# Kernel optimization log

Hardware: AMD Instinct MI355X
Metric: run time of the kernel (lower is better)

## Reference

```python
import jax, jax.numpy as jnp
import numpy as np

ALPHA = 0.2  # leaky relu slope
NEG_INF = -9e15

B, N, F_IN, F_OUT = 2, 4096, 256, 256
EMB = 16  # int(sqrt(256))


def setup_inputs() -> dict:
    key = jax.random.key(0)
    ks = jax.random.split(key, 16)
    g = 1.414

    def xavier(k, shape):
        fan_in, fan_out = shape[0], shape[1]
        limit = g * np.sqrt(6.0 / (fan_in + fan_out))
        return jax.random.uniform(k, shape, jnp.float32, -limit, limit)

    feat = jax.random.normal(ks[0], (B, N, F_IN), jnp.float32)
    adj = jax.random.randint(ks[1], (B, N, N), 0, 2, jnp.int32)
    W = xavier(ks[2], (F_IN, F_OUT))
    a1 = xavier(ks[3], (F_OUT, 1))
    a2 = xavier(ks[4], (F_OUT, 1))
    a12 = xavier(ks[5], (F_OUT, F_OUT))
    # BiInteraction linear layers stored as [in, out] (= torch weight.T)
    def lin(k1, k2, fi, fo):
        lim = 1.0 / np.sqrt(fi)
        w = jax.random.uniform(k1, (fi, fo), jnp.float32, -lim, lim)
        b = jax.random.uniform(k2, (fo,), jnp.float32, -lim, lim)
        return w, b

    e1_w, e1_b = lin(ks[6], ks[7], F_IN, EMB)
    e2_w, e2_b = lin(ks[8], ks[9], F_IN, EMB)
    i0_w, i0_b = lin(ks[10], ks[11], 2 * EMB, F_OUT)
    i1_w, i1_b = lin(ks[12], ks[13], F_OUT, F_OUT)
    return {"feat": feat, "adj": adj, "W": W, "a1": a1, "a2": a2,
            "a12": a12, "e1_w": e1_w, "e1_b": e1_b, "e2_w": e2_w,
            "e2_b": e2_b, "i0_w": i0_w, "i0_b": i0_b, "i1_w": i1_w,
            "i1_b": i1_b}


def reference(feat, adj, W, a1, a2, a12, e1_w, e1_b, e2_w, e2_b,
              i0_w, i0_b, i1_w, i1_b):
    lrelu = lambda x: jax.nn.leaky_relu(x, ALPHA)
    # attention scores: logits[b,i,j] = a1.h_j + a2.h_i + h_i A12 h_j
    h = feat @ W                                   # [B,N,F_OUT]
    Ax = (h @ a1).transpose(0, 2, 1)               # [B,1,N] (key term)
    Ay = h @ a2                                    # [B,N,1] (query term)
    Axy = jnp.einsum('bnd,de,bme->bnm', h, a12, h) # [B,N,N] bilinear
    e = lrelu(Ax + Ay + Axy)
    e = jnp.where(adj > 0, e, NEG_INF)
    attention = jax.nn.softmax(e, axis=-1)         # masked softmax over j
    h_prime = attention @ feat                     # [B,N,F_IN]
    # BiInteraction MLP update
    emb1 = lrelu(feat @ e1_w + e1_b)
    emb2 = lrelu(h_prime @ e2_w + e2_b)
    c = jnp.concatenate([emb1, emb2], axis=-1)     # [B,N,2*EMB]
    c = lrelu(c @ i0_w + i0_b)
    c = lrelu(c @ i1_w + i1_b)
    return c
```

## Files before the change

kernel.cpp:

```cpp
#include <hip/hip_runtime.h>
#include <hip/hip_bf16.h>

typedef __attribute__((ext_vector_type(8))) __bf16 bf16x8;
typedef __attribute__((ext_vector_type(8))) short short8;
typedef __attribute__((ext_vector_type(4))) float floatx4;
typedef __attribute__((ext_vector_type(4))) int intx4;
typedef unsigned short u16;
typedef unsigned int u32;
typedef unsigned long long u64;

constexpr int BB = 2, NN = 4096, DD = 256;
constexpr int NCHUNK = 4;
constexpr int KSTEP = 32;
constexpr int CHUNKLEN = NN / NCHUNK;
constexpr int STEPS = CHUNKLEN / KSTEP;
constexpr float SLOPE = 0.2f;
constexpr float NEGINF = -9e15f;

#define DEVI static __device__ __forceinline__

DEVI u16 f2bf(float f) {
  u32 u = __float_as_uint(f);
  u += 0x7fffu + ((u >> 16) & 1u);
  return (u16)(u >> 16);
}
DEVI float bf2f(u16 h) { return __uint_as_float(((u32)h) << 16); }
DEVI float lrelu(float x) { return x > 0.f ? x : SLOPE * x; }

DEVI floatx4 mfma16(short8 a, short8 b, floatx4 c) {
  return __builtin_amdgcn_mfma_f32_16x16x32_bf16(
      __builtin_bit_cast(bf16x8, a), __builtin_bit_cast(bf16x8, b), c, 0, 0, 0);
}

__global__ void k_prep_w(const float* W, const float* A12, const float* I1,
                         u16* WThi, u16* WTlo, u16* A12Thi, u16* A12Tlo,
                         u16* I1Thi, u16* I1Tlo) {
  __shared__ float tile[32][33];
  const float* src = blockIdx.z == 0 ? W : (blockIdx.z == 1 ? A12 : I1);
  u16* dhi = blockIdx.z == 0 ? WThi : (blockIdx.z == 1 ? A12Thi : I1Thi);
  u16* dlo = blockIdx.z == 0 ? WTlo : (blockIdx.z == 1 ? A12Tlo : I1Tlo);
  int k0 = blockIdx.x * 32, n0 = blockIdx.y * 32;
  int tx = threadIdx.x, ty = threadIdx.y;
  #pragma unroll
  for (int r = 0; r < 4; r++)
    tile[ty + r * 8][tx] = src[(size_t)(k0 + ty + r * 8) * 256 + n0 + tx];
  __syncthreads();
  #pragma unroll
  for (int r = 0; r < 4; r++) {
    float v = tile[tx][ty + r * 8];
    u16 hb = f2bf(v);
    size_t o = (size_t)(n0 + ty + r * 8) * 256 + k0 + tx;
    dhi[o] = hb;
    dlo[o] = f2bf(v - bf2f(hb));
  }
}

__global__ void k_prep_e(const float* e1w, const float* e2w, float* e1t,
                         float* e2t) {
  int t = threadIdx.x;
  const float* src = blockIdx.x == 0 ? e1w : e2w;
  float* dst = blockIdx.x == 0 ? e1t : e2t;
  float v[16];
  #pragma unroll
  for (int o = 0; o < 16; o++) v[o] = src[t * 16 + o];
  #pragma unroll
  for (int o = 0; o < 16; o++) dst[o * 256 + t] = v[o];
}

__global__ void k_adjpack(const int* adj, u64* maskp) {
  int wave = (blockIdx.x * 256 + threadIdx.x) >> 6;
  int lane = threadIdx.x & 63;
  size_t base = (size_t)wave * 256;
  const int* p = adj + base;
  u64 m[4];
  #pragma unroll
  for (int r = 0; r < 4; r++) {
    int v = p[r * 64 + lane];
    m[r] = __ballot(v > 0);
  }
  if (lane < 4) {
    u64 sel = lane == 0 ? m[0] : lane == 1 ? m[1] : lane == 2 ? m[2] : m[3];
    maskp[base / 64 + lane] = sel;
  }
}

template <int AMODE, int EPI>
__global__ __launch_bounds__(256) void k_gemm(
    const float* Af32, const u16* Ahi, const u16* Alo,
    const u16* BThi, const u16* BTlo,
    u16* Ohi, u16* Olo, float* Of32, const float* bias) {
  int t = threadIdx.x;
  int wid = t >> 6, lane = t & 63;
  int li = lane & 15, lg = lane >> 4;
  int row0 = blockIdx.x * 64 + wid * 16;
  int col0 = blockIdx.y * 32;
  int arow = row0 + li;

  __shared__ __align__(16) u16 Bh[32 * 256];
  __shared__ __align__(16) u16 Bl[32 * 256];
  #pragma unroll
  for (int s = 0; s < 4; s++) {
    int r = s * 8 + (t >> 5), c8 = (t & 31) * 8;
    int off = r * 256 + (c8 ^ ((r & 7) << 3));
    *(intx4*)(Bh + off) = *(const intx4*)(BThi + (size_t)(col0 + r) * DD + c8);
    *(intx4*)(Bl + off) = *(const intx4*)(BTlo + (size_t)(col0 + r) * DD + c8);
  }

  short8 ahi[8], alo[8];
  if constexpr (AMODE == 0) {
    const float* ap = Af32 + (size_t)arow * DD + lg * 8;
    #pragma unroll
    for (int ks = 0; ks < 8; ks++) {
      floatx4 f0 = *(const floatx4*)(ap + ks * 32);
      floatx4 f1 = *(const floatx4*)(ap + ks * 32 + 4);
      short8 h, l;
      #pragma unroll
      for (int e = 0; e < 4; e++) {
        u16 hb = f2bf(f0[e]); h[e] = (short)hb; l[e] = (short)f2bf(f0[e] - bf2f(hb));
        u16 hb2 = f2bf(f1[e]); h[e + 4] = (short)hb2; l[e + 4] = (short)f2bf(f1[e] - bf2f(hb2));
      }
      ahi[ks] = h; alo[ks] = l;
    }
  } else {
    const u16* ap = Ahi + (size_t)arow * DD + lg * 8;
    const u16* ap2 = Alo + (size_t)arow * DD + lg * 8;
    #pragma unroll
    for (int ks = 0; ks < 8; ks++) {
      ahi[ks] = *(const short8*)(ap + ks * 32);
      alo[ks] = *(const short8*)(ap2 + ks * 32);
    }
  }
  __syncthreads();

  floatx4 acc[2];
  #pragma unroll
  for (int cf = 0; cf < 2; cf++) acc[cf] = 0.f;

  #pragma unroll
  for (int cf = 0; cf < 2; cf++) {
    int row = cf * 16 + li;
    int rsw = (row & 7) << 3;
    #pragma unroll
    for (int ks = 0; ks < 8; ks++) {
      int off = row * 256 + ((ks * 32 + lg * 8) ^ rsw);
      short8 bhf = *(const short8*)(Bh + off);
      short8 blf = *(const short8*)(Bl + off);
      acc[cf] = mfma16(ahi[ks], bhf, acc[cf]);
      acc[cf] = mfma16(alo[ks], bhf, acc[cf]);
      acc[cf] = mfma16(ahi[ks], blf, acc[cf]);
    }
  }

  #pragma unroll
  for (int cf = 0; cf < 2; cf++) {
    int col = col0 + cf * 16 + li;
    #pragma unroll
    for (int r = 0; r < 4; r++) {
      int row = row0 + lg * 4 + r;
      float v = acc[cf][r];
      if constexpr (EPI == 0) {
        u16 hb = f2bf(v);
        Ohi[(size_t)row * DD + col] = hb;
        Olo[(size_t)row * DD + col] = f2bf(v - bf2f(hb));
      } else {
        v += bias[col];
        v = lrelu(v);
        Of32[(size_t)row * DD + col] = v;
      }
    }
  }
}

__global__ void k_axay(const u16* h_hi, const u16* h_lo, const float* a1,
                       const float* a2, float* ax, float* ay) {
  int row = blockIdx.x * 4 + (threadIdx.x >> 6);
  int lane = threadIdx.x & 63;
  ushort4 hw = *(const ushort4*)(h_hi + (size_t)row * DD + lane * 4);
  ushort4 lw = *(const ushort4*)(h_lo + (size_t)row * DD + lane * 4);
  floatx4 av1 = *(const floatx4*)(a1 + lane * 4);
  floatx4 av2 = *(const floatx4*)(a2 + lane * 4);
  const u16* hp = (const u16*)&hw;
  const u16* lp = (const u16*)&lw;
  float s1 = 0.f, s2 = 0.f;
  #pragma unroll
  for (int r = 0; r < 4; r++) {
    float hv = bf2f(hp[r]) + bf2f(lp[r]);
    s1 += hv * av1[r];
    s2 += hv * av2[r];
  }
  #pragma unroll
  for (int off = 32; off; off >>= 1) {
    s1 += __shfl_xor(s1, off);
    s2 += __shfl_xor(s2, off);
  }
  if (lane == 0) { ax[row] = s1; ay[row] = s2; }
}

__global__ void k_featT(const float* feat, u16* featT) {
  __shared__ float tile[64][65];
  int b = blockIdx.z, n0 = blockIdx.x * 64, d0 = blockIdx.y * 64;
  int tx = threadIdx.x & 63, ty = threadIdx.x >> 6;
  #pragma unroll
  for (int r = 0; r < 16; r++) {
    int n = ty + r * 4;
    tile[n][tx] = feat[((size_t)b * NN + n0 + n) * DD + d0 + tx];
  }
  __syncthreads();
  #pragma unroll
  for (int r = 0; r < 16; r++) {
    int d = ty + r * 4;
    featT[((size_t)b * DD + d0 + d) * NN + n0 + tx] = f2bf(tile[tx][d]);
  }
}

__global__ __launch_bounds__(256, 2) void k_flash(
    const u16* t_hi, const u16* t_lo, const u16* h_hi, const u16* h_lo,
    const u16* featT, const float* ax, const float* ay, const u64* maskp,
    float* PO, float* m_ws, float* l_ws) {
  int id = blockIdx.x;
  int wg = (id & 7) * 64 + (id >> 3);
  int b = wg >> 8;
  int rem = wg & 255;
  int chunk = rem >> 6;
  int it = rem & 63;

  int t = threadIdx.x;
  int wid = t >> 6, lane = t & 63;
  int li = lane & 15, lg = lane >> 4;
  int i = it * 64 + wid * 16 + li;
  size_t browQ = (size_t)b * NN + i;

  __shared__ __align__(16) u16 Kh[KSTEP * 256];
  __shared__ __align__(16) u16 Kl[KSTEP * 256];
  __shared__ __align__(16) u16 Vs[256 * KSTEP];
  __shared__ __align__(16) u16 Pbuf[4][16][40];

  short8 qhi[8], qlo[8];
  {
    const u16* qp = t_hi + browQ * DD + lg * 8;
    const u16* qp2 = t_lo + browQ * DD + lg * 8;
    #pragma unroll
    for (int ks = 0; ks < 8; ks++) {
      qhi[ks] = *(const short8*)(qp + ks * 32);
      qlo[ks] = *(const short8*)(qp2 + ks * 32);
    }
  }
  float ayv = ay[browQ];
  const float* axp = ax + (size_t)b * NN;
  const u32* mrow = (const u32*)maskp + browQ * (NN / 32);
  const u16* kh_src = h_hi + ((size_t)b * NN + chunk * CHUNKLEN) * DD;
  const u16* kl_src = h_lo + ((size_t)b * NN + chunk * CHUNKLEN) * DD;
  const u16* v_src = featT + (size_t)b * DD * NN + chunk * CHUNKLEN;

  floatx4 acc[16];
  #pragma unroll
  for (int df = 0; df < 16; df++) acc[df] = 0.f;
  float m_run = -INFINITY, l_run = 0.f;

  intx4 sKh[4], sKl[4], sVv[4];
  {
    int r = (t >> 5), c8 = (t & 31) * 8;
    int dv = (t >> 2), cv = (t & 3) * 8;
    #pragma unroll
    for (int s = 0; s < 4; s++) {
      sKh[s] = *(const intx4*)(kh_src + (size_t)(s * 8 + r) * DD + c8);
      sKl[s] = *(const intx4*)(kl_src + (size_t)(s * 8 + r) * DD + c8);
      sVv[s] = *(const intx4*)(v_src + (size_t)(s * 64 + dv) * NN + cv);
    }
  }

  for (int jt = 0; jt < STEPS; jt++) {
    __syncthreads();
    {
      int r0 = (t >> 5), c8 = (t & 31) * 8;
      int dv0 = (t >> 2), cv = (t & 3) * 8;
      #pragma unroll
      for (int s = 0; s < 4; s++) {
        int r = s * 8 + r0;
        int off = r * 256 + (c8 ^ ((r & 7) << 3));
        *(intx4*)(Kh + off) = sKh[s];
        *(intx4*)(Kl + off) = sKl[s];
        int d = s * 64 + dv0;
        *(intx4*)(Vs + d * KSTEP + (cv ^ (((d >> 1) & 3) << 3))) = sVv[s];
      }
    }
    __syncthreads();
    int j0 = jt * KSTEP;
    if (jt + 1 < STEPS) {
      const u16* kh2 = kh_src + (size_t)(j0 + KSTEP) * DD;
      const u16* kl2 = kl_src + (size_t)(j0 + KSTEP) * DD;
      int r = (t >> 5), c8 = (t & 31) * 8;
      int dv = (t >> 2), cv = (t & 3) * 8;
      #pragma unroll
      for (int s = 0; s < 4; s++) {
        sKh[s] = *(const intx4*)(kh2 + (size_t)(s * 8 + r) * DD + c8);
        sKl[s] = *(const intx4*)(kl2 + (size_t)(s * 8 + r) * DD + c8);
        sVv[s] = *(const intx4*)(v_src + (size_t)(s * 64 + dv) * NN + (j0 + KSTEP) + cv);
      }
    }

    int ja = chunk * CHUNKLEN + j0;
    u32 M = mrow[ja >> 5];
    floatx4 axv[2];
    axv[0] = *(const floatx4*)(axp + ja + lg * 4);
    axv[1] = *(const floatx4*)(axp + ja + 16 + lg * 4);

    floatx4 sacc[2];
    sacc[0] = 0.f; sacc[1] = 0.f;
    #pragma unroll
    for (int ks = 0; ks < 8; ks++) {
      #pragma unroll
      for (int fi = 0; fi < 2; fi++) {
        int row = fi * 16 + li;
        int off = row * 256 + ((ks * 32 + lg * 8) ^ ((row & 7) << 3));
        short8 a0 = *(const short8*)(Kh + off);
        short8 a1 = *(const short8*)(Kl + off);
        sacc[fi] = mfma16(a0, qhi[ks], sacc[fi]);
        sacc[fi] = mfma16(a1, qhi[ks], sacc[fi]);
        sacc[fi] = mfma16(a0, qlo[ks], sacc[fi]);
      }
    }
    float sv[2][4];
    float m_tile = -INFINITY;
    #pragma unroll
    for (int fi = 0; fi < 2; fi++) {
      u32 nib = (M >> (fi * 16 + lg * 4)) & 0xFu;
      #pragma unroll
      for (int r = 0; r < 4; r++) {
        float s = sacc[fi][r] + axv[fi][r] + ayv;
        s = lrelu(s);
        s = (nib >> r) & 1u ? s : NEGINF;
        sv[fi][r] = s;
        m_tile = fmaxf(m_tile, s);
      }
    }
    m_tile = fmaxf(m_tile, __shfl_xor(m_tile, 16));
    m_tile = fmaxf(m_tile, __shfl_xor(m_tile, 32));
    bool nores = __all(m_tile <= m_run);
    if (!nores) {
      float m_new = fmaxf(m_run, m_tile);
      float scale = __expf(m_run - m_new);
      l_run *= scale;
      #pragma unroll
      for (int df = 0; df < 16; df++) acc[df] *= scale;
      m_run = m_new;
    }

    float psum = 0.f;
    #pragma unroll
    for (int fi = 0; fi < 2; fi++) {
      u16 pb[4];
      #pragma unroll
      for (int r = 0; r < 4; r++) {
        float p = __expf(sv[fi][r] - m_run);
        pb[r] = f2bf(p);
        psum += bf2f(pb[r]);
      }
      u32 w0 = (u32)pb[0] | ((u32)pb[1] << 16);
      u32 w1 = (u32)pb[2] | ((u32)pb[3] << 16);
      *(uint2*)&Pbuf[wid][li][fi * 16 + lg * 4] = make_uint2(w0, w1);
    }
    psum += __shfl_xor(psum, 16);
    psum += __shfl_xor(psum, 32);
    l_run += psum;

    short8 pf = *(const short8*)&Pbuf[wid][li][lg * 8];
    #pragma unroll
    for (int df = 0; df < 16; df++) {
      int d = df * 16 + li;
      short8 vf = *(const short8*)(Vs + d * KSTEP + ((lg * 8) ^ (((d >> 1) & 3) << 3)));
      acc[df] = mfma16(vf, pf, acc[df]);
    }
  }

  size_t pobase = ((size_t)(b * NCHUNK + chunk) * NN + i) * DD;
  #pragma unroll
  for (int df = 0; df < 16; df++)
    *(floatx4*)(PO + pobase + df * 16 + lg * 4) = acc[df];
  if (lg == 0) {
    size_t mi = ((size_t)b * NCHUNK + chunk) * NN + i;
    m_ws[mi] = m_run;
    l_ws[mi] = l_run;
  }
}

__global__ void k_combine_mlp(const float* PO, const float* m_ws,
                              const float* l_ws, const float* feat,
                              const float* e1t, const float* e1b,
                              const float* e2t, const float* e2b,
                              const float* i0w, const float* i0b,
                              u16* c_hi, u16* c_lo) {
  int b = blockIdx.y;
  int t = threadIdx.x;
  int i = blockIdx.x * 4 + (t >> 6);
  int lane = t & 63;
  int d4 = lane * 4;
  size_t row = (size_t)b * NN + i;

  float mc[NCHUNK], lc[NCHUNK];
  #pragma unroll
  for (int c = 0; c < NCHUNK; c++) {
    mc[c] = m_ws[((size_t)b * NCHUNK + c) * NN + i];
    lc[c] = l_ws[((size_t)b * NCHUNK + c) * NN + i];
  }
  float M = -INFINITY;
  #pragma unroll
  for (int c = 0; c < NCHUNK; c++) M = fmaxf(M, mc[c]);
  float w[NCHUNK], L = 0.f;
  #pragma unroll
  for (int c = 0; c < NCHUNK; c++) { w[c] = __expf(mc[c] - M); L += w[c] * lc[c]; }
  float invL = 1.f / L;

  floatx4 hv = 0.f;
  #pragma unroll
  for (int c = 0; c < NCHUNK; c++) {
    floatx4 v = *(const floatx4*)(PO + ((size_t)(b * NCHUNK + c) * NN + i) * DD + d4);
    hv += w[c] * v;
  }
  hv *= invL;

  floatx4 fv = *(const floatx4*)(feat + row * DD + d4);
  float p1[16], p2[16];
  #pragma unroll
  for (int o = 0; o < 16; o++) {
    floatx4 w1 = *(const floatx4*)(e1t + o * 256 + d4);
    floatx4 w2 = *(const floatx4*)(e2t + o * 256 + d4);
    p1[o] = fv[0] * w1[0] + fv[1] * w1[1] + fv[2] * w1[2] + fv[3] * w1[3];
    p2[o] = hv[0] * w2[0] + hv[1] * w2[1] + hv[2] * w2[2] + hv[3] * w2[3];
  }
  #pragma unroll
  for (int off = 32; off; off >>= 1) {
    #pragma unroll
    for (int o = 0; o < 16; o++) {
      p1[o] += __shfl_xor(p1[o], off);
      p2[o] += __shfl_xor(p2[o], off);
    }
  }
  float cc[32];
  #pragma unroll
  for (int o = 0; o < 16; o++) {
    cc[o] = lrelu(p1[o] + e1b[o]);
    cc[16 + o] = lrelu(p2[o] + e2b[o]);
  }
  #pragma unroll
  for (int q = 0; q < 4; q++) {
    int o2 = q * 64 + lane;
    float s = i0b[o2];
    #pragma unroll
    for (int k = 0; k < 32; k++) s += cc[k] * i0w[(size_t)k * 256 + o2];
    s = lrelu(s);
    u16 hb = f2bf(s);
    c_hi[row * DD + o2] = hb;
    c_lo[row * DD + o2] = f2bf(s - bf2f(hb));
  }
}

extern "C" void kernel_launch(void* const* d_in, const int* in_sizes, int n_in,
                              void* d_out, int out_size, void* d_ws,
                              size_t ws_size, hipStream_t stream) {
  const float* feat = (const float*)d_in[0];
  const int* adj = (const int*)d_in[1];
  const float* W = (const float*)d_in[2];
  const float* a1 = (const float*)d_in[3];
  const float* a2 = (const float*)d_in[4];
  const float* a12 = (const float*)d_in[5];
  const float* e1w = (const float*)d_in[6];
  const float* e1b = (const float*)d_in[7];
  const float* e2w = (const float*)d_in[8];
  const float* e2b = (const float*)d_in[9];
  const float* i0w = (const float*)d_in[10];
  const float* i0b = (const float*)d_in[11];
  const float* i1w = (const float*)d_in[12];
  const float* i1b = (const float*)d_in[13];
  float* out = (float*)d_out;

  char* p = (char*)d_ws;
  auto carve = [&](size_t bytes) -> char* {
    char* r = p;
    p += (bytes + 255) & ~(size_t)255;
    return r;
  };
  const size_t MAT = 256 * 256 * sizeof(u16);
  const size_t BND = (size_t)BB * NN * DD * sizeof(u16);
  u16* WThi = (u16*)carve(MAT);
  u16* WTlo = (u16*)carve(MAT);
  u16* A12Thi = (u16*)carve(MAT);
  u16* A12Tlo = (u16*)carve(MAT);
  u16* I1Thi = (u16*)carve(MAT);
  u16* I1Tlo = (u16*)carve(MAT);
  u16* h_hi = (u16*)carve(BND);
  u16* h_lo = (u16*)carve(BND);
  u16* t_hi = (u16*)carve(BND);
  u16* t_lo = (u16*)carve(BND);
  u16* featT = (u16*)carve(BND);
  float* ax = (float*)carve((size_t)BB * NN * 4);
  float* ay = (float*)carve((size_t)BB * NN * 4);
  u64* maskp = (u64*)carve((size_t)BB * NN * (NN / 64) * 8);
  float* PO = (float*)carve((size_t)BB * NCHUNK * NN * DD * 4);
  float* m_ws = (float*)carve((size_t)BB * NCHUNK * NN * 4);
  float* l_ws = (float*)carve((size_t)BB * NCHUNK * NN * 4);
  float* e1t = (float*)carve(256 * 16 * 4);
  float* e2t = (float*)carve(256 * 16 * 4);
  u16* c_hi = (u16*)carve(BND);
  u16* c_lo = (u16*)carve(BND);

  k_adjpack<<<32768, 256, 0, stream>>>(adj, maskp);
  k_prep_w<<<dim3(8, 8, 3), dim3(32, 8), 0, stream>>>(
      W, a12, i1w, WThi, WTlo, A12Thi, A12Tlo, I1Thi, I1Tlo);
  k_prep_e<<<2, 256, 0, stream>>>(e1w, e2w, e1t, e2t);
  k_gemm<0, 0><<<dim3(128, 8), 256, 0, stream>>>(
      feat, nullptr, nullptr, WThi, WTlo, h_hi, h_lo, nullptr, nullptr);
  k_axay<<<2048, 256, 0, stream>>>(h_hi, h_lo, a1, a2, ax, ay);
  k_gemm<1, 0><<<dim3(128, 8), 256, 0, stream>>>(
      nullptr, h_hi, h_lo, A12Thi, A12Tlo, t_hi, t_lo, nullptr, nullptr);
  k_featT<<<dim3(64, 4, 2), 256, 0, stream>>>(feat, featT);
  k_flash<<<512, 256, 0, stream>>>(
      t_hi, t_lo, h_hi, h_lo, featT, ax, ay, maskp, PO, m_ws, l_ws);
  k_combine_mlp<<<dim3(1024, 2), 256, 0, stream>>>(
      PO, m_ws, l_ws, feat, e1t, e1b, e2t, e2b, i0w, i0b, c_hi, c_lo);
  k_gemm<1, 1><<<dim3(128, 8), 256, 0, stream>>>(
      nullptr, c_hi, c_lo, I1Thi, I1Tlo, nullptr, nullptr, out, i1b);
}
```

Before: 387.0 us.

## Fuse query bilinear projection into flash kernel and merge prep launches

Drops the separate GEMM that computed t = h·A12 into global memory. Each flash workgroup now computes its own query rows of t with MFMA from h and A12, then splits them into bf16 hi/lo parts through shared memory before the attention loop. Separately, the e1/e2 transposes are folded into the weight-prep kernel, and the adjacency packing uses fewer blocks that each loop over 16 waves. This saves two kernel launches and a round trip of t through HBM, but it repeats the t projection once per key chunk (four times) and adds a shared-memory staging phase to each flash block.

```diff
diff --git a/kernel.cpp b/kernel.cpp
--- a/kernel.cpp
+++ b/kernel.cpp
@@ -33,8 +33,22 @@
 }
 
 __global__ void k_prep_w(const float* W, const float* A12, const float* I1,
+                         const float* e1w, const float* e2w,
                          u16* WThi, u16* WTlo, u16* A12Thi, u16* A12Tlo,
-                         u16* I1Thi, u16* I1Tlo) {
+                         u16* I1Thi, u16* I1Tlo, float* e1t, float* e2t) {
+  if (blockIdx.z == 3) {
+    if (blockIdx.x < 2 && blockIdx.y == 0) {
+      int t = threadIdx.y * 32 + threadIdx.x;
+      const float* src = blockIdx.x == 0 ? e1w : e2w;
+      float* dst = blockIdx.x == 0 ? e1t : e2t;
+      float v[16];
+      #pragma unroll
+      for (int o = 0; o < 16; o++) v[o] = src[t * 16 + o];
+      #pragma unroll
+      for (int o = 0; o < 16; o++) dst[o * 256 + t] = v[o];
+    }
+    return;
+  }
   __shared__ float tile[32][33];
   const float* src = blockIdx.z == 0 ? W : (blockIdx.z == 1 ? A12 : I1);
   u16* dhi = blockIdx.z == 0 ? WThi : (blockIdx.z == 1 ? A12Thi : I1Thi);
@@ -55,32 +69,23 @@
   }
 }
 
-__global__ void k_prep_e(const float* e1w, const float* e2w, float* e1t,
-                         float* e2t) {
-  int t = threadIdx.x;
-  const float* src = blockIdx.x == 0 ? e1w : e2w;
-  float* dst = blockIdx.x == 0 ? e1t : e2t;
-  float v[16];
-  #pragma unroll
-  for (int o = 0; o < 16; o++) v[o] = src[t * 16 + o];
-  #pragma unroll
-  for (int o = 0; o < 16; o++) dst[o * 256 + t] = v[o];
-}
-
 __global__ void k_adjpack(const int* adj, u64* maskp) {
-  int wave = (blockIdx.x * 256 + threadIdx.x) >> 6;
+  int wv0 = (blockIdx.x * 256 + threadIdx.x) >> 6;
   int lane = threadIdx.x & 63;
-  size_t base = (size_t)wave * 256;
-  const int* p = adj + base;
-  u64 m[4];
-  #pragma unroll
-  for (int r = 0; r < 4; r++) {
-    int v = p[r * 64 + lane];
-    m[r] = __ballot(v > 0);
-  }
-  if (lane < 4) {
-    u64 sel = lane == 0 ? m[0] : lane == 1 ? m[1] : lane == 2 ? m[2] : m[3];
-    maskp[base / 64 + lane] = sel;
+  for (int g = 0; g < 16; g++) {
+    int wave = wv0 + g * 8192;
+    size_t base = (size_t)wave * 256;
+    const int* p = adj + base;
+    u64 m[4];
+    #pragma unroll
+    for (int r = 0; r < 4; r++) {
+      int v = p[r * 64 + lane];
+      m[r] = __ballot(v > 0);
+    }
+    if (lane < 4) {
+      u64 sel = lane == 0 ? m[0] : lane == 1 ? m[1] : lane == 2 ? m[2] : m[3];
+      maskp[base / 64 + lane] = sel;
+    }
   }
 }
 
@@ -214,7 +219,7 @@
 }
 
 __global__ __launch_bounds__(256, 2) void k_flash(
-    const u16* t_hi, const u16* t_lo, const u16* h_hi, const u16* h_lo,
+    const u16* h_hi, const u16* h_lo, const u16* A12Thi, const u16* A12Tlo,
     const u16* featT, const float* ax, const float* ay, const u64* maskp,
     float* PO, float* m_ws, float* l_ws) {
   int id = blockIdx.x;
@@ -230,32 +235,16 @@
   int i = it * 64 + wid * 16 + li;
   size_t browQ = (size_t)b * NN + i;
 
-  __shared__ __align__(16) u16 Kh[KSTEP * 256];
-  __shared__ __align__(16) u16 Kl[KSTEP * 256];
-  __shared__ __align__(16) u16 Vs[256 * KSTEP];
+  __shared__ __align__(16) u16 SMEM[3 * KSTEP * 256];
+  u16* Kh = SMEM;
+  u16* Kl = SMEM + KSTEP * 256;
+  u16* Vs = SMEM + 2 * KSTEP * 256;
+  u16* TT = SMEM;
   __shared__ __align__(16) u16 Pbuf[4][16][40];
 
-  short8 qhi[8], qlo[8];
-  {
-    const u16* qp = t_hi + browQ * DD + lg * 8;
-    const u16* qp2 = t_lo + browQ * DD + lg * 8;
-    #pragma unroll
-    for (int ks = 0; ks < 8; ks++) {
-      qhi[ks] = *(const short8*)(qp + ks * 32);
-      qlo[ks] = *(const short8*)(qp2 + ks * 32);
-    }
-  }
-  float ayv = ay[browQ];
-  const float* axp = ax + (size_t)b * NN;
-  const u32* mrow = (const u32*)maskp + browQ * (NN / 32);
   const u16* kh_src = h_hi + ((size_t)b * NN + chunk * CHUNKLEN) * DD;
   const u16* kl_src = h_lo + ((size_t)b * NN + chunk * CHUNKLEN) * DD;
   const u16* v_src = featT + (size_t)b * DD * NN + chunk * CHUNKLEN;
-
-  floatx4 acc[16];
-  #pragma unroll
-  for (int df = 0; df < 16; df++) acc[df] = 0.f;
-  float m_run = -INFINITY, l_run = 0.f;
 
   intx4 sKh[4], sKl[4], sVv[4];
   {
@@ -268,6 +257,74 @@
       sVv[s] = *(const intx4*)(v_src + (size_t)(s * 64 + dv) * NN + cv);
     }
   }
+
+  floatx4 acc[16];
+  short8 qhi[8], qlo[8];
+
+  {
+    const u16* hp = h_hi + browQ * DD + lg * 8;
+    const u16* hp2 = h_lo + browQ * DD + lg * 8;
+    #pragma unroll
+    for (int ks = 0; ks < 8; ks++) {
+      qhi[ks] = *(const short8*)(hp + ks * 32);
+      qlo[ks] = *(const short8*)(hp2 + ks * 32);
+    }
+    #pragma unroll
+    for (int cf = 0; cf < 16; cf++) {
+      floatx4 ta = 0.f;
+      const u16* aph = A12Thi + (size_t)(cf * 16 + li) * DD + lg * 8;
+      const u16* apl = A12Tlo + (size_t)(cf * 16 + li) * DD + lg * 8;
+      #pragma unroll
+      for (int ks = 0; ks < 8; ks++) {
+        short8 w0 = *(const short8*)(aph + ks * 32);
+        short8 w1 = *(const short8*)(apl + ks * 32);
+        ta = mfma16(w0, qhi[ks], ta);
+        ta = mfma16(w1, qhi[ks], ta);
+        ta = mfma16(w0, qlo[ks], ta);
+      }
+      acc[cf] = ta;
+    }
+    int trow = wid * 16 + li;
+    int tsw = (li & 7) << 3;
+    #pragma unroll
+    for (int cf = 0; cf < 16; cf++) {
+      u16 hb[4];
+      #pragma unroll
+      for (int r = 0; r < 4; r++) {
+        hb[r] = f2bf(acc[cf][r]);
+        acc[cf][r] = acc[cf][r] - bf2f(hb[r]);
+      }
+      *(uint2*)&TT[trow * 256 + ((cf * 16 + lg * 4) ^ tsw)] =
+          make_uint2((u32)hb[0] | ((u32)hb[1] << 16),
+                     (u32)hb[2] | ((u32)hb[3] << 16));
+    }
+    __syncthreads();
+    #pragma unroll
+    for (int ks = 0; ks < 8; ks++)
+      qhi[ks] = *(const short8*)(&TT[trow * 256 + ((ks * 32 + lg * 8) ^ tsw)]);
+    __syncthreads();
+    #pragma unroll
+    for (int cf = 0; cf < 16; cf++) {
+      u16 lb[4];
+      #pragma unroll
+      for (int r = 0; r < 4; r++) lb[r] = f2bf(acc[cf][r]);
+      *(uint2*)&TT[trow * 256 + ((cf * 16 + lg * 4) ^ tsw)] =
+          make_uint2((u32)lb[0] | ((u32)lb[1] << 16),
+                     (u32)lb[2] | ((u32)lb[3] << 16));
+    }
+    __syncthreads();
+    #pragma unroll
+    for (int ks = 0; ks < 8; ks++)
+      qlo[ks] = *(const short8*)(&TT[trow * 256 + ((ks * 32 + lg * 8) ^ tsw)]);
+  }
+
+  float ayv = ay[browQ];
+  const float* axp = ax + (size_t)b * NN;
+  const u32* mrow = (const u32*)maskp + browQ * (NN / 32);
+
+  #pragma unroll
+  for (int df = 0; df < 16; df++) acc[df] = 0.f;
+  float m_run = -INFINITY, l_run = 0.f;
 
   for (int jt = 0; jt < STEPS; jt++) {
     __syncthreads();
@@ -490,8 +547,6 @@
   u16* I1Tlo = (u16*)carve(MAT);
   u16* h_hi = (u16*)carve(BND);
   u16* h_lo = (u16*)carve(BND);
-  u16* t_hi = (u16*)carve(BND);
-  u16* t_lo = (u16*)carve(BND);
   u16* featT = (u16*)carve(BND);
   float* ax = (float*)carve((size_t)BB * NN * 4);
   float* ay = (float*)carve((size_t)BB * NN * 4);
@@ -504,18 +559,16 @@
   u16* c_hi = (u16*)carve(BND);
   u16* c_lo = (u16*)carve(BND);
 
-  k_adjpack<<<32768, 256, 0, stream>>>(adj, maskp);
-  k_prep_w<<<dim3(8, 8, 3), dim3(32, 8), 0, stream>>>(
-      W, a12, i1w, WThi, WTlo, A12Thi, A12Tlo, I1Thi, I1Tlo);
-  k_prep_e<<<2, 256, 0, stream>>>(e1w, e2w, e1t, e2t);
+  k_adjpack<<<2048, 256, 0, stream>>>(adj, maskp);
+  k_prep_w<<<dim3(8, 8, 4), dim3(32, 8), 0, stream>>>(
+      W, a12, i1w, e1w, e2w, WThi, WTlo, A12Thi, A12Tlo, I1Thi, I1Tlo,
+      e1t, e2t);
   k_gemm<0, 0><<<dim3(128, 8), 256, 0, stream>>>(
       feat, nullptr, nullptr, WThi, WTlo, h_hi, h_lo, nullptr, nullptr);
   k_axay<<<2048, 256, 0, stream>>>(h_hi, h_lo, a1, a2, ax, ay);
-  k_gemm<1, 0><<<dim3(128, 8), 256, 0, stream>>>(
-      nullptr, h_hi, h_lo, A12Thi, A12Tlo, t_hi, t_lo, nullptr, nullptr);
   k_featT<<<dim3(64, 4, 2), 256, 0, stream>>>(feat, featT);
   k_flash<<<512, 256, 0, stream>>>(
-      t_hi, t_lo, h_hi, h_lo, featT, ax, ay, maskp, PO, m_ws, l_ws);
+      h_hi, h_lo, A12Thi, A12Tlo, featT, ax, ay, maskp, PO, m_ws, l_ws);
   k_combine_mlp<<<dim3(1024, 2), 256, 0, stream>>>(
       PO, m_ws, l_ws, feat, e1t, e1b, e2t, e2b, i0w, i0b, c_hi, c_lo);
   k_gemm<1, 1><<<dim3(128, 8), 256, 0, stream>>>(
```

Result: slower. 433.3 us (+12.0%).
